# Performance work log

Measured on AMD Instinct MI355X. Metric: run time of the kernel, lower is better.

Reference implementation:

```python
import jax, jax.numpy as jnp
import numpy as np

N = 100000
E = 1600000
H = 128
L = 5
G = 128
OUT = 128
BN_EPS = 1e-5


def setup_inputs() -> dict:
    key = jax.random.key(0)
    ks = jax.random.split(key, 16)
    x = jax.random.randint(ks[0], (N,), 0, 1)
    edge_index = jax.random.randint(ks[1], (2, E), 0, N)
    edge_attr = jax.random.normal(ks[2], (E, 7), dtype=jnp.float32)
    batch = jnp.sort(jax.random.randint(ks[3], (N,), 0, G))
    s = 0.05
    node_emb = jax.random.normal(ks[4], (1, H), dtype=jnp.float32) * s
    W = jax.random.normal(ks[5], (L, H, H), dtype=jnp.float32) * s
    b = jnp.zeros((L, H), dtype=jnp.float32)
    We = jax.random.normal(ks[6], (L, 7, H), dtype=jnp.float32) * s
    be = jnp.zeros((L, H), dtype=jnp.float32)
    root = jax.random.normal(ks[7], (L, 1, H), dtype=jnp.float32) * s
    gamma = jnp.ones((L, H), dtype=jnp.float32)
    beta = jnp.zeros((L, H), dtype=jnp.float32)
    Wout = jax.random.normal(ks[8], (H, OUT), dtype=jnp.float32) * s
    bout = jnp.zeros((OUT,), dtype=jnp.float32)
    return {"x": x, "edge_index": edge_index, "edge_attr": edge_attr, "batch": batch,
            "node_emb": node_emb, "W": W, "b": b, "We": We, "be": be, "root": root,
            "gamma": gamma, "beta": beta, "Wout": Wout, "bout": bout}


def _batchnorm(h, g, bta):
    mu = jnp.mean(h, axis=0)
    var = jnp.var(h, axis=0)  # biased, as torch BN training normalization
    return (h - mu) * jax.lax.rsqrt(var + BN_EPS) * g + bta


def reference(x, edge_index, edge_attr, batch, node_emb, W, b, We, be, root, gamma, beta, Wout, bout):
    row, col = edge_index[0], edge_index[1]
    # degree(row) + 1
    deg = jax.ops.segment_sum(jnp.ones((E,), edge_attr.dtype), row, num_segments=N) + 1.0
    dis = deg ** -0.5  # never inf since deg >= 1
    norm = dis[row] * dis[col]  # [E]

    h = node_emb[x]  # [N, H]
    for i in range(L):
        xl = h @ W[i] + b[i]                    # [N, H]
        e = edge_attr @ We[i] + be[i]           # [E, H]
        msg = norm[:, None] * jax.nn.relu(xl[row] + e)   # [E, H]
        agg = jax.ops.segment_sum(msg, col, num_segments=N)
        h = agg + jax.nn.relu(xl + root[i]) / deg[:, None]
        h = _batchnorm(h, gamma[i], beta[i])
        if i < L - 1:
            h = jax.nn.relu(h)
    # global mean pool
    cnt = jax.ops.segment_sum(jnp.ones((N,), h.dtype), batch, num_segments=G)
    hg = jax.ops.segment_sum(h, batch, num_segments=G) / jnp.maximum(cnt, 1.0)[:, None]
    return hg @ Wout + bout
```

## Files before the change

kernel.cpp:

```cpp
#include <hip/hip_runtime.h>
#include <hip/hip_fp16.h>
#include <cstdint>
#include <cstddef>

#define N_NODES 100000
#define N_EDGES 1600000
#define H 128
#define L_LAYERS 5
#define G_GRAPHS 128
#define OUT_F 128
#define BN_EPS 1e-5f
#define SCAN_BLOCKS 98

typedef _Float16 half8_t __attribute__((ext_vector_type(8)));
typedef float floatx4 __attribute__((ext_vector_type(4)));

__device__ __forceinline__ float frelu(float x) { return fmaxf(x, 0.0f); }


__global__ void count_kernel(const int* __restrict__ erow, const int* __restrict__ ecol,
                             int* __restrict__ degcnt, int* __restrict__ hist) {
    int e = blockIdx.x * 256 + threadIdx.x;
    atomicAdd(&degcnt[erow[e]], 1);
    atomicAdd(&hist[ecol[e]], 1);
}

__global__ void finish_deg(const int* __restrict__ degcnt, float* __restrict__ dis,
                           float* __restrict__ invdeg) {
    int i = blockIdx.x * 256 + threadIdx.x;
    if (i < N_NODES) {
        float d = (float)degcnt[i] + 1.0f;
        dis[i] = rsqrtf(d);
        invdeg[i] = 1.0f / d;
    }
}

__global__ __launch_bounds__(1024) void scan_part(const int* __restrict__ hist,
                                                  int* __restrict__ rowptr,
                                                  int* __restrict__ blocksum) {
    int t = threadIdx.x;
    int i = blockIdx.x * 1024 + t;
    int orig = (i < N_NODES) ? hist[i] : 0;
    int v = orig;
#pragma unroll
    for (int off = 1; off < 64; off <<= 1) {
        int u = __shfl_up(v, off);
        if ((t & 63) >= off) v += u;
    }
    __shared__ int wsum[16];
    int wid = t >> 6;
    if ((t & 63) == 63) wsum[wid] = v;
    __syncthreads();
    int woff = 0;
#pragma unroll
    for (int w = 0; w < 16; w++)
        if (w < wid) woff += wsum[w];
    int incl = v + woff;
    if (i < N_NODES) rowptr[i] = incl - orig;
    if (t == 1023) blocksum[blockIdx.x] = incl;
}

__global__ __launch_bounds__(128) void scan_block(const int* __restrict__ blocksum,
                                                  int* __restrict__ blockoff,
                                                  int* __restrict__ rowptr) {
    int t = threadIdx.x;
    int orig = (t < SCAN_BLOCKS) ? blocksum[t] : 0;
    int v = orig;
#pragma unroll
    for (int off = 1; off < 64; off <<= 1) {
        int u = __shfl_up(v, off);
        if ((t & 63) >= off) v += u;
    }
    __shared__ int w0;
    if (t == 63) w0 = v;
    __syncthreads();
    if (t >= 64) v += w0;
    if (t < SCAN_BLOCKS) blockoff[t] = v - orig;
    if (t == 0) rowptr[N_NODES] = N_EDGES;
}

__global__ __launch_bounds__(1024) void scan_add(int* __restrict__ rowptr,
                                                 const int* __restrict__ blockoff,
                                                 int* __restrict__ cursor) {
    int i = blockIdx.x * 1024 + threadIdx.x;
    if (i < N_NODES) {
        int v = rowptr[i] + blockoff[blockIdx.x];
        rowptr[i] = v;
        cursor[i] = v;
    }
}

__global__ void scatter_kernel(const int* __restrict__ erow, const int* __restrict__ ecol,
                               const float* __restrict__ ea, const float* __restrict__ dis,
                               int* __restrict__ cursor,
                               float* __restrict__ ea8, int* __restrict__ rows) {
    int e = blockIdx.x * 256 + threadIdx.x;
    int c = ecol[e];
    int r = erow[e];
    float nrm = dis[r] * dis[c];
    int pos = atomicAdd(&cursor[c], 1);
    const float* p = ea + (size_t)e * 7;
    float a0 = p[0], a1 = p[1], a2 = p[2], a3 = p[3], a4 = p[4], a5 = p[5], a6 = p[6];
    float* dst = ea8 + (size_t)pos * 8;
    *(float4*)dst = make_float4(a0, a1, a2, a3);
    *(float4*)(dst + 4) = make_float4(a4, a5, a6, nrm);
    rows[pos] = r;
}

__global__ __launch_bounds__(256) void gemm_xl(const __half* __restrict__ hsrc,
                                               const int* __restrict__ xidx,
                                               const float* __restrict__ nemb,
                                               const float* __restrict__ colsum_p,
                                               const float* __restrict__ colsumsq_p,
                                               const float* __restrict__ gamma_p,
                                               const float* __restrict__ beta_p,
                                               const float* __restrict__ Wl,
                                               const float* __restrict__ bl,
                                               __half* __restrict__ xlo, int mode) {
    __shared__ half8_t sB[2048];
    __shared__ float sScale[H], sShift[H];
    int t = threadIdx.x;
    if (mode == 1 && t < H) {
        float mean = colsum_p[t] * (1.0f / N_NODES);
        float var = colsumsq_p[t] * (1.0f / N_NODES) - mean * mean;
        float s = gamma_p[t] * rsqrtf(var + BN_EPS);
        sScale[t] = s;
        sShift[t] = beta_p[t] - mean * s;
    }
    for (int idx = t; idx < 2048; idx += 256) {
        int ct = idx >> 8;
        int ks = (idx >> 6) & 3;
        int ln = idx & 63;
        int kbase = ks * 32 + (ln >> 4) * 8;
        int c = ct * 16 + (ln & 15);
        half8_t v;
#pragma unroll
        for (int i = 0; i < 8; i++)
            v[i] = (_Float16)Wl[(size_t)(kbase + i) * H + c];
        sB[idx] = v;
    }
    __syncthreads();

    int w = t >> 6, lane = t & 63;
    int lq = lane >> 4, lr = lane & 15;
    int rbase = blockIdx.x * 128 + w * 32;

    floatx4 acc[2][8];
#pragma unroll
    for (int rt = 0; rt < 2; rt++)
#pragma unroll
        for (int ct = 0; ct < 8; ct++) acc[rt][ct] = (floatx4)0.0f;

    float bias[8];
#pragma unroll
    for (int ct = 0; ct < 8; ct++) bias[ct] = bl[ct * 16 + lr];

    int arow[2], xv[2];
#pragma unroll
    for (int rt = 0; rt < 2; rt++) {
        int row = rbase + rt * 16 + lr;
        if (row > N_NODES - 1) row = N_NODES - 1;
        arow[rt] = row;
        if (mode == 0) xv[rt] = xidx[row];
    }

    for (int ks = 0; ks < 4; ks++) {
        int k0 = ks * 32 + lq * 8;
        half8_t a[2];
#pragma unroll
        for (int rt = 0; rt < 2; rt++) {
            float f[8];
            if (mode == 0) {
                const float* p = nemb + (size_t)xv[rt] * H + k0;
                float4 u0 = *(const float4*)p;
                float4 u1 = *(const float4*)(p + 4);
                f[0] = u0.x; f[1] = u0.y; f[2] = u0.z; f[3] = u0.w;
                f[4] = u1.x; f[5] = u1.y; f[6] = u1.z; f[7] = u1.w;
            } else {
                union { float4 f4; __half2 h2[4]; } u;
                u.f4 = *(const float4*)(hsrc + (size_t)arow[rt] * H + k0);
#pragma unroll
                for (int i = 0; i < 4; i++) {
                    float2 d = __half22float2(u.h2[i]);
                    f[2 * i] = d.x; f[2 * i + 1] = d.y;
                }
#pragma unroll
                for (int i = 0; i < 8; i++)
                    f[i] = frelu(f[i] * sScale[k0 + i] + sShift[k0 + i]);
            }
            half8_t av;
#pragma unroll
            for (int i = 0; i < 8; i++) av[i] = (_Float16)f[i];
            a[rt] = av;
        }
#pragma unroll
        for (int ct = 0; ct < 8; ct++) {
            half8_t bf = sB[(ct * 4 + ks) * 64 + lane];
            acc[0][ct] = __builtin_amdgcn_mfma_f32_16x16x32_f16(a[0], bf, acc[0][ct], 0, 0, 0);
            acc[1][ct] = __builtin_amdgcn_mfma_f32_16x16x32_f16(a[1], bf, acc[1][ct], 0, 0, 0);
        }
    }

#pragma unroll
    for (int rt = 0; rt < 2; rt++)
#pragma unroll
        for (int ct = 0; ct < 8; ct++)
#pragma unroll
            for (int r = 0; r < 4; r++) {
                int row = rbase + rt * 16 + lq * 4 + r;
                if (row < N_NODES)
                    xlo[(size_t)row * H + ct * 16 + lr] =
                        __float2half(acc[rt][ct][r] + bias[ct]);
            }
}

__global__ __launch_bounds__(256) void agg_kernel(
    const int* __restrict__ rowptr, const float* __restrict__ ea8,
    const int* __restrict__ rows, const __half2* __restrict__ xh2,
    const float* __restrict__ invdeg, const float* __restrict__ rootl,
    const float* __restrict__ Wel, const float* __restrict__ bel,
    __half2* __restrict__ hpreh, float* __restrict__ colsum,
    float* __restrict__ colsumsq) {
    int t = threadIdx.x;
    int lane = t & 63, wv = t >> 6;
    int c0 = lane * 2;
    float w00 = Wel[0 * H + c0], w01 = Wel[0 * H + c0 + 1];
    float w10 = Wel[1 * H + c0], w11 = Wel[1 * H + c0 + 1];
    float w20 = Wel[2 * H + c0], w21 = Wel[2 * H + c0 + 1];
    float w30 = Wel[3 * H + c0], w31 = Wel[3 * H + c0 + 1];
    float w40 = Wel[4 * H + c0], w41 = Wel[4 * H + c0 + 1];
    float w50 = Wel[5 * H + c0], w51 = Wel[5 * H + c0 + 1];
    float w60 = Wel[6 * H + c0], w61 = Wel[6 * H + c0 + 1];
    float be0 = bel[c0], be1 = bel[c0 + 1];
    float rt0 = rootl[c0], rt1 = rootl[c0 + 1];
    float s0 = 0, s1 = 0, q0 = 0, q1 = 0;

#define MLP_BODY(V0, V1, XG)                                                 \
    {                                                                        \
        float2 xg_ = __half22float2(XG);                                     \
        float m0_ = be0, m1_ = be1;                                          \
        m0_ = fmaf((V0).x, w00, m0_); m1_ = fmaf((V0).x, w01, m1_);          \
        m0_ = fmaf((V0).y, w10, m0_); m1_ = fmaf((V0).y, w11, m1_);          \
        m0_ = fmaf((V0).z, w20, m0_); m1_ = fmaf((V0).z, w21, m1_);          \
        m0_ = fmaf((V0).w, w30, m0_); m1_ = fmaf((V0).w, w31, m1_);          \
        m0_ = fmaf((V1).x, w40, m0_); m1_ = fmaf((V1).x, w41, m1_);          \
        m0_ = fmaf((V1).y, w50, m0_); m1_ = fmaf((V1).y, w51, m1_);          \
        m0_ = fmaf((V1).z, w60, m0_); m1_ = fmaf((V1).z, w61, m1_);          \
        a0 = fmaf(frelu(xg_.x + m0_), (V1).w, a0);                           \
        a1 = fmaf(frelu(xg_.y + m1_), (V1).w, a1);                           \
    }

    for (int n_ = blockIdx.x * 4 + wv; n_ < N_NODES; n_ += gridDim.x * 4) {
        int n = __builtin_amdgcn_readfirstlane(n_);
        int jb = __builtin_amdgcn_readfirstlane(rowptr[n]);
        int je = __builtin_amdgcn_readfirstlane(rowptr[n + 1]);
        float a0 = 0, a1 = 0;
        int j = jb;
        for (; j + 8 <= je; j += 8) {
            int rr[8];
#pragma unroll
            for (int i = 0; i < 8; i++) rr[i] = rows[j + i];
            __half2 g[8];
#pragma unroll
            for (int i = 0; i < 8; i++) g[i] = xh2[(size_t)rr[i] * 64 + lane];
#pragma unroll
            for (int i = 0; i < 8; i++) {
                const float* ep_ = ea8 + (size_t)(j + i) * 8;
                float4 va = *(const float4*)ep_, vb = *(const float4*)(ep_ + 4);
                MLP_BODY(va, vb, g[i]);
            }
        }
        if (j + 4 <= je) {
            int rr[4];
#pragma unroll
            for (int i = 0; i < 4; i++) rr[i] = rows[j + i];
            __half2 g[4];
#pragma unroll
            for (int i = 0; i < 4; i++) g[i] = xh2[(size_t)rr[i] * 64 + lane];
#pragma unroll
            for (int i = 0; i < 4; i++) {
                const float* ep_ = ea8 + (size_t)(j + i) * 8;
                float4 va = *(const float4*)ep_, vb = *(const float4*)(ep_ + 4);
                MLP_BODY(va, vb, g[i]);
            }
            j += 4;
        }
        for (; j < je; j++) {
            int r_ = rows[j];
            const float* ep_ = ea8 + (size_t)j * 8;
            float4 va = *(const float4*)ep_, vb = *(const float4*)(ep_ + 4);
            __half2 g_ = xh2[(size_t)r_ * 64 + lane];
            MLP_BODY(va, vb, g_);
        }
        float2 xn = __half22float2(xh2[(size_t)n * 64 + lane]);
        float id = invdeg[n];
        float p0 = a0 + frelu(xn.x + rt0) * id;
        float p1 = a1 + frelu(xn.y + rt1) * id;
        hpreh[(size_t)n * 64 + lane] = __float22half2_rn(make_float2(p0, p1));
        s0 += p0; s1 += p1;
        q0 = fmaf(p0, p0, q0); q1 = fmaf(p1, p1, q1);
    }
#undef MLP_BODY

    __shared__ float red[4][H];
    red[wv][c0] = s0; red[wv][c0 + 1] = s1;
    __syncthreads();
    if (wv == 0) {
        float t0 = red[0][c0] + red[1][c0] + red[2][c0] + red[3][c0];
        float t1 = red[0][c0 + 1] + red[1][c0 + 1] + red[2][c0 + 1] + red[3][c0 + 1];
        unsafeAtomicAdd(&colsum[c0], t0);
        unsafeAtomicAdd(&colsum[c0 + 1], t1);
    }
    __syncthreads();
    red[wv][c0] = q0; red[wv][c0 + 1] = q1;
    __syncthreads();
    if (wv == 0) {
        float t0 = red[0][c0] + red[1][c0] + red[2][c0] + red[3][c0];
        float t1 = red[0][c0 + 1] + red[1][c0 + 1] + red[2][c0 + 1] + red[3][c0 + 1];
        unsafeAtomicAdd(&colsumsq[c0], t0);
        unsafeAtomicAdd(&colsumsq[c0 + 1], t1);
    }
}

__global__ __launch_bounds__(256) void pool_kernel(const __half2* __restrict__ hh,
                                                   const int* __restrict__ batch,
                                                   const float* __restrict__ colsum_p,
                                                   const float* __restrict__ colsumsq_p,
                                                   const float* __restrict__ gamma_p,
                                                   const float* __restrict__ beta_p,
                                                   float* __restrict__ pooled,
                                                   float* __restrict__ cnt) {
    __shared__ float sScale[H], sShift[H];
    int t = threadIdx.x;
    if (t < H) {
        float mean = colsum_p[t] * (1.0f / N_NODES);
        float var = colsumsq_p[t] * (1.0f / N_NODES) - mean * mean;
        float s = gamma_p[t] * rsqrtf(var + BN_EPS);
        sScale[t] = s;
        sShift[t] = beta_p[t] - mean * s;
    }
    __syncthreads();
    int cg = t & 63, rg = t >> 6;
    int c0 = cg * 2;
    float sc0 = sScale[c0], sc1 = sScale[c0 + 1];
    float sh0 = sShift[c0], sh1 = sShift[c0 + 1];
    int per = (N_NODES + gridDim.x - 1) / gridDim.x;
    int rstart = blockIdx.x * per;
    int rend = min(rstart + per, N_NODES);
    float a0 = 0, a1 = 0, runc = 0.0f;
    int cur = -1;
    for (int rowi = rstart + rg; rowi < rend; rowi += 4) {
        int g = batch[rowi];
        if (g != cur) {
            if (cur >= 0) {
                unsafeAtomicAdd(&pooled[(size_t)cur * H + c0 + 0], a0);
                unsafeAtomicAdd(&pooled[(size_t)cur * H + c0 + 1], a1);
                if (cg == 0) unsafeAtomicAdd(&cnt[cur], runc);
            }
            cur = g; a0 = 0; a1 = 0; runc = 0.0f;
        }
        float2 v = __half22float2(hh[(size_t)rowi * 64 + cg]);
        a0 += v.x * sc0 + sh0;
        a1 += v.y * sc1 + sh1;
        runc += 1.0f;
    }
    if (cur >= 0) {
        unsafeAtomicAdd(&pooled[(size_t)cur * H + c0 + 0], a0);
        unsafeAtomicAdd(&pooled[(size_t)cur * H + c0 + 1], a1);
        if (cg == 0) unsafeAtomicAdd(&cnt[cur], runc);
    }
}

__global__ __launch_bounds__(128) void final_gemm(const float* __restrict__ pooled,
                                                  const float* __restrict__ cnt,
                                                  const float* __restrict__ Wout,
                                                  const float* __restrict__ bout,
                                                  float* __restrict__ out) {
    __shared__ float sh[H];
    int g = blockIdx.x;
    int o = threadIdx.x;
    float c = fmaxf(cnt[g], 1.0f);
    sh[o] = pooled[(size_t)g * H + o] / c;
    __syncthreads();
    float acc = bout[o];
#pragma unroll 8
    for (int k = 0; k < H; k++) acc += sh[k] * Wout[(size_t)k * OUT_F + o];
    out[(size_t)g * OUT_F + o] = acc;
}

extern "C" void kernel_launch(void* const* d_in, const int* in_sizes, int n_in,
                              void* d_out, int out_size, void* d_ws, size_t ws_size,
                              hipStream_t stream) {
    const int*   x     = (const int*)d_in[0];
    const int*   ei    = (const int*)d_in[1];
    const float* ea    = (const float*)d_in[2];
    const int*   batch = (const int*)d_in[3];
    const float* nemb  = (const float*)d_in[4];
    const float* W     = (const float*)d_in[5];
    const float* b     = (const float*)d_in[6];
    const float* We    = (const float*)d_in[7];
    const float* be    = (const float*)d_in[8];
    const float* root  = (const float*)d_in[9];
    const float* gamma = (const float*)d_in[10];
    const float* beta  = (const float*)d_in[11];
    const float* Wout  = (const float*)d_in[12];
    const float* bout  = (const float*)d_in[13];
    float* out = (float*)d_out;

    const int* erow = ei;
    const int* ecol = ei + N_EDGES;

    float* ws = (float*)d_ws;
    size_t NH = (size_t)N_NODES * H;
    float* ea8    = ws;
    int*   rows   = (int*)(ea8 + (size_t)N_EDGES * 8);
    float* hslot  = (float*)(rows + N_EDGES);
    __half* hpreh = (__half*)hslot;
    float* xslot  = hslot + NH / 2;
    __half* xlh   = (__half*)xslot;
    int*   rowptr = (int*)(xslot + NH / 2);
    float* dis    = (float*)(rowptr + N_NODES + 4);
    float* invdeg = dis + N_NODES;
    float* colsumAll = invdeg + N_NODES;
    float* pooled   = colsumAll + (size_t)L_LAYERS * 2 * H;
    float* cnt      = pooled + (size_t)G_GRAPHS * H;
    int*   blocksum = (int*)(cnt + G_GRAPHS);
    int*   blockoff = blocksum + 128;

    int* degcnt = (int*)hslot;
    int* hist   = degcnt + N_NODES;
    int* cursor = hist + N_NODES;

    hipMemsetAsync(degcnt, 0, 2 * N_NODES * sizeof(int), stream);
    hipMemsetAsync(colsumAll, 0, (size_t)L_LAYERS * 2 * H * sizeof(float), stream);
    hipLaunchKernelGGL(count_kernel, dim3(N_EDGES / 256), dim3(256), 0, stream,
                       erow, ecol, degcnt, hist);
    hipLaunchKernelGGL(finish_deg, dim3((N_NODES + 255) / 256), dim3(256), 0, stream,
                       degcnt, dis, invdeg);
    hipLaunchKernelGGL(scan_part, dim3(SCAN_BLOCKS), dim3(1024), 0, stream,
                       hist, rowptr, blocksum);
    hipLaunchKernelGGL(scan_block, dim3(1), dim3(128), 0, stream,
                       blocksum, blockoff, rowptr);
    hipLaunchKernelGGL(scan_add, dim3(SCAN_BLOCKS), dim3(1024), 0, stream,
                       rowptr, blockoff, cursor);
    hipLaunchKernelGGL(scatter_kernel, dim3(N_EDGES / 256), dim3(256), 0, stream,
                       erow, ecol, ea, dis, cursor, ea8, rows);

    for (int l = 0; l < L_LAYERS; l++) {
        const float* cs_prev = colsumAll + (size_t)(l - 1) * 2 * H;
        hipLaunchKernelGGL(gemm_xl, dim3((N_NODES + 127) / 128), dim3(256), 0, stream,
                           hpreh, x, nemb,
                           (l == 0) ? colsumAll : cs_prev,
                           (l == 0) ? colsumAll : cs_prev + H,
                           gamma + (size_t)(l ? l - 1 : 0) * H,
                           beta + (size_t)(l ? l - 1 : 0) * H,
                           W + (size_t)l * H * H, b + (size_t)l * H, xlh,
                           (l == 0) ? 0 : 1);
        float* cs = colsumAll + (size_t)l * 2 * H;
        hipLaunchKernelGGL(agg_kernel, dim3(2048), dim3(256), 0, stream,
                           rowptr, ea8, rows, (const __half2*)xlh, invdeg,
                           root + (size_t)l * H, We + (size_t)l * 7 * H, be + (size_t)l * H,
                           (__half2*)hpreh, cs, cs + H);
    }

    hipMemsetAsync(pooled, 0, ((size_t)G_GRAPHS * H + G_GRAPHS) * sizeof(float), stream);
    {
        const float* cs4 = colsumAll + (size_t)(L_LAYERS - 1) * 2 * H;
        hipLaunchKernelGGL(pool_kernel, dim3(256), dim3(256), 0, stream,
                           (const __half2*)hpreh, batch, cs4, cs4 + H,
                           gamma + (size_t)(L_LAYERS - 1) * H,
                           beta + (size_t)(L_LAYERS - 1) * H, pooled, cnt);
    }
    hipLaunchKernelGGL(final_gemm, dim3(G_GRAPHS), dim3(OUT_F), 0, stream,
                       pooled, cnt, Wout, bout, out);
}
```

Before: 1.365 ms.

## Assign contiguous node ranges per wave and software-pipeline edge gathers across nodes

The aggregation kernel now gives each wavefront a contiguous run of 13 nodes and walks their edges as one flat stream. It double-buffers the row indices and gathered xl features in batches of 8, prefetching the next batch while the current one is processed. A flush step emits each node's result at its boundary and prefetches the next node's self features. This removes per-node loop overhead and the serial tails for low-degree nodes, and keeps more gathers in flight, at the cost of more registers and per-edge boundary checks. 2048 blocks × 4 waves × 13 nodes covers all 100000 nodes.

```diff
diff --git a/kernel.cpp b/kernel.cpp
--- a/kernel.cpp
+++ b/kernel.cpp
@@ -11,6 +11,8 @@
 #define OUT_F 128
 #define BN_EPS 1e-5f
 #define SCAN_BLOCKS 98
+#define AGG_BLOCKS 2048
+#define NPW 13
 
 typedef _Float16 half8_t __attribute__((ext_vector_type(8)));
 typedef float floatx4 __attribute__((ext_vector_type(4)));
@@ -235,6 +237,27 @@
     float rt0 = rootl[c0], rt1 = rootl[c0 + 1];
     float s0 = 0, s1 = 0, q0 = 0, q1 = 0;
 
+    int wgid = blockIdx.x * 4 + wv;
+    int n0 = wgid * NPW;
+    bool active = (n0 < N_NODES);
+    int n1 = active ? min(n0 + NPW, N_NODES) : n0;
+    int n = n0;
+    float a0 = 0, a1 = 0;
+
+    __half2 xn_cur = __half2{}, xn_next = __half2{};
+    float idg_cur = 0, idg_next = 0;
+    int je = 0, e0 = 0, e1 = 0;
+    if (active) {
+        e0 = __builtin_amdgcn_readfirstlane(rowptr[n0]);
+        e1 = __builtin_amdgcn_readfirstlane(rowptr[n1]);
+        je = __builtin_amdgcn_readfirstlane(rowptr[n0 + 1]);
+        xn_cur = xh2[(size_t)n0 * 64 + lane];
+        idg_cur = invdeg[n0];
+        int nx = min(n0 + 1, N_NODES - 1);
+        xn_next = xh2[(size_t)nx * 64 + lane];
+        idg_next = invdeg[nx];
+    }
+
 #define MLP_BODY(V0, V1, XG)                                                 \
     {                                                                        \
         float2 xg_ = __half22float2(XG);                                     \
@@ -250,56 +273,87 @@
         a1 = fmaf(frelu(xg_.y + m1_), (V1).w, a1);                           \
     }
 
-    for (int n_ = blockIdx.x * 4 + wv; n_ < N_NODES; n_ += gridDim.x * 4) {
-        int n = __builtin_amdgcn_readfirstlane(n_);
-        int jb = __builtin_amdgcn_readfirstlane(rowptr[n]);
-        int je = __builtin_amdgcn_readfirstlane(rowptr[n + 1]);
-        float a0 = 0, a1 = 0;
-        int j = jb;
-        for (; j + 8 <= je; j += 8) {
-            int rr[8];
-#pragma unroll
-            for (int i = 0; i < 8; i++) rr[i] = rows[j + i];
-            __half2 g[8];
-#pragma unroll
-            for (int i = 0; i < 8; i++) g[i] = xh2[(size_t)rr[i] * 64 + lane];
-#pragma unroll
-            for (int i = 0; i < 8; i++) {
-                const float* ep_ = ea8 + (size_t)(j + i) * 8;
-                float4 va = *(const float4*)ep_, vb = *(const float4*)(ep_ + 4);
-                MLP_BODY(va, vb, g[i]);
+#define FLUSH()                                                              \
+    {                                                                        \
+        float2 xnf_ = __half22float2(xn_cur);                                \
+        float p0_ = a0 + frelu(xnf_.x + rt0) * idg_cur;                      \
+        float p1_ = a1 + frelu(xnf_.y + rt1) * idg_cur;                      \
+        hpreh[(size_t)n * 64 + lane] = __float22half2_rn(make_float2(p0_, p1_)); \
+        s0 += p0_; s1 += p1_;                                                \
+        q0 = fmaf(p0_, p0_, q0); q1 = fmaf(p1_, p1_, q1);                    \
+        a0 = 0; a1 = 0;                                                      \
+        xn_cur = xn_next; idg_cur = idg_next;                                \
+        int nn_ = min(n + 2, N_NODES - 1);                                   \
+        xn_next = xh2[(size_t)nn_ * 64 + lane];                              \
+        idg_next = invdeg[nn_];                                              \
+    }
+
+#define PROCESS(G)                                                           \
+    {                                                                        \
+        _Pragma("unroll")                                                    \
+        for (int i = 0; i < 8; i++) {                                        \
+            int jj = j + i;                                                  \
+            if (jj < e1) {                                                   \
+                while (jj >= je) {                                           \
+                    FLUSH();                                                 \
+                    n++;                                                     \
+                    je = __builtin_amdgcn_readfirstlane(rowptr[n + 1]);      \
+                }                                                            \
+                const float* ep_ = ea8 + (size_t)jj * 8;                     \
+                float4 va_ = *(const float4*)ep_;                            \
+                float4 vb_ = *(const float4*)(ep_ + 4);                      \
+                MLP_BODY(va_, vb_, G[i]);                                    \
+            }                                                                \
+        }                                                                    \
+    }
+
+    if (active && e1 > e0) {
+        int rrA[8], rrB[8];
+        __half2 gA[8], gB[8];
+        int eclamp = e1 - 1;
+#pragma unroll
+        for (int i = 0; i < 8; i++)
+            rrA[i] = __builtin_amdgcn_readfirstlane(rows[min(e0 + i, eclamp)]);
+#pragma unroll
+        for (int i = 0; i < 8; i++) gA[i] = xh2[(size_t)rrA[i] * 64 + lane];
+#pragma unroll
+        for (int i = 0; i < 8; i++)
+            rrB[i] = __builtin_amdgcn_readfirstlane(rows[min(e0 + 8 + i, eclamp)]);
+
+        int j = e0;
+        while (true) {
+            if (j >= e1) break;
+            {
+                if (j + 8 < e1) {
+#pragma unroll
+                    for (int i = 0; i < 8; i++) gB[i] = xh2[(size_t)rrB[i] * 64 + lane];
+#pragma unroll
+                    for (int i = 0; i < 8; i++)
+                        rrA[i] = __builtin_amdgcn_readfirstlane(rows[min(j + 16 + i, eclamp)]);
+                }
+                PROCESS(gA);
+                j += 8;
+            }
+            if (j >= e1) break;
+            {
+                if (j + 8 < e1) {
+#pragma unroll
+                    for (int i = 0; i < 8; i++) gA[i] = xh2[(size_t)rrA[i] * 64 + lane];
+#pragma unroll
+                    for (int i = 0; i < 8; i++)
+                        rrB[i] = __builtin_amdgcn_readfirstlane(rows[min(j + 16 + i, eclamp)]);
+                }
+                PROCESS(gB);
+                j += 8;
             }
         }
-        if (j + 4 <= je) {
-            int rr[4];
-#pragma unroll
-            for (int i = 0; i < 4; i++) rr[i] = rows[j + i];
-            __half2 g[4];
-#pragma unroll
-            for (int i = 0; i < 4; i++) g[i] = xh2[(size_t)rr[i] * 64 + lane];
-#pragma unroll
-            for (int i = 0; i < 4; i++) {
-                const float* ep_ = ea8 + (size_t)(j + i) * 8;
-                float4 va = *(const float4*)ep_, vb = *(const float4*)(ep_ + 4);
-                MLP_BODY(va, vb, g[i]);
-            }
-            j += 4;
-        }
-        for (; j < je; j++) {
-            int r_ = rows[j];
-            const float* ep_ = ea8 + (size_t)j * 8;
-            float4 va = *(const float4*)ep_, vb = *(const float4*)(ep_ + 4);
-            __half2 g_ = xh2[(size_t)r_ * 64 + lane];
-            MLP_BODY(va, vb, g_);
-        }
-        float2 xn = __half22float2(xh2[(size_t)n * 64 + lane]);
-        float id = invdeg[n];
-        float p0 = a0 + frelu(xn.x + rt0) * id;
-        float p1 = a1 + frelu(xn.y + rt1) * id;
-        hpreh[(size_t)n * 64 + lane] = __float22half2_rn(make_float2(p0, p1));
-        s0 += p0; s1 += p1;
-        q0 = fmaf(p0, p0, q0); q1 = fmaf(p1, p1, q1);
-    }
+    }
+    while (n < n1) {
+        FLUSH();
+        n++;
+    }
+#undef PROCESS
+#undef FLUSH
 #undef MLP_BODY
 
     __shared__ float red[4][H];
@@ -457,7 +511,7 @@
                            W + (size_t)l * H * H, b + (size_t)l * H, xlh,
                            (l == 0) ? 0 : 1);
         float* cs = colsumAll + (size_t)l * 2 * H;
-        hipLaunchKernelGGL(agg_kernel, dim3(2048), dim3(256), 0, stream,
+        hipLaunchKernelGGL(agg_kernel, dim3(AGG_BLOCKS), dim3(256), 0, stream,
                            rowptr, ea8, rows, (const __half2*)xlh, invdeg,
                            root + (size_t)l * H, We + (size_t)l * 7 * H, be + (size_t)l * H,
                            (__half2*)hpreh, cs, cs + H);
```

After: 1.724 ms. 1.26x slower.

## Pack edge attributes and norm into fp16, unroll aggregation loop to 16

Applied to the files above, without the earlier changes.

Edge attributes and the normalization factor are stored as eight fp16 values (16 bytes per edge) instead of eight fp32 values, halving the per-edge stream the aggregation kernel reads on every layer. The aggregation loop also adds a 16-edge unrolled stage so more neighbor-row gathers are in flight at once. The cost is fp16 rounding of edge features and norm, which lowers accuracy, plus higher register pressure from the wider unroll.

```diff
diff --git a/kernel.cpp b/kernel.cpp
--- a/kernel.cpp
+++ b/kernel.cpp
@@ -93,17 +93,19 @@
 __global__ void scatter_kernel(const int* __restrict__ erow, const int* __restrict__ ecol,
                                const float* __restrict__ ea, const float* __restrict__ dis,
                                int* __restrict__ cursor,
-                               float* __restrict__ ea8, int* __restrict__ rows) {
+                               float4* __restrict__ eah, int* __restrict__ rows) {
     int e = blockIdx.x * 256 + threadIdx.x;
     int c = ecol[e];
     int r = erow[e];
     float nrm = dis[r] * dis[c];
     int pos = atomicAdd(&cursor[c], 1);
     const float* p = ea + (size_t)e * 7;
-    float a0 = p[0], a1 = p[1], a2 = p[2], a3 = p[3], a4 = p[4], a5 = p[5], a6 = p[6];
-    float* dst = ea8 + (size_t)pos * 8;
-    *(float4*)dst = make_float4(a0, a1, a2, a3);
-    *(float4*)(dst + 4) = make_float4(a4, a5, a6, nrm);
+    union { float4 f4; __half2 h2[4]; } u;
+    u.h2[0] = __float22half2_rn(make_float2(p[0], p[1]));
+    u.h2[1] = __float22half2_rn(make_float2(p[2], p[3]));
+    u.h2[2] = __float22half2_rn(make_float2(p[4], p[5]));
+    u.h2[3] = __float22half2_rn(make_float2(p[6], nrm));
+    eah[pos] = u.f4;
     rows[pos] = r;
 }
 
@@ -215,7 +217,7 @@
 }
 
 __global__ __launch_bounds__(256) void agg_kernel(
-    const int* __restrict__ rowptr, const float* __restrict__ ea8,
+    const int* __restrict__ rowptr, const float4* __restrict__ eah,
     const int* __restrict__ rows, const __half2* __restrict__ xh2,
     const float* __restrict__ invdeg, const float* __restrict__ rootl,
     const float* __restrict__ Wel, const float* __restrict__ bel,
@@ -235,19 +237,24 @@
     float rt0 = rootl[c0], rt1 = rootl[c0 + 1];
     float s0 = 0, s1 = 0, q0 = 0, q1 = 0;
 
-#define MLP_BODY(V0, V1, XG)                                                 \
+#define MLP_BODY(PV, XG)                                                     \
     {                                                                        \
+        const __half2* ph_ = (const __half2*)&(PV);                          \
+        float2 A01_ = __half22float2(ph_[0]);                                \
+        float2 A23_ = __half22float2(ph_[1]);                                \
+        float2 A45_ = __half22float2(ph_[2]);                                \
+        float2 A6N_ = __half22float2(ph_[3]);                                \
         float2 xg_ = __half22float2(XG);                                     \
         float m0_ = be0, m1_ = be1;                                          \
-        m0_ = fmaf((V0).x, w00, m0_); m1_ = fmaf((V0).x, w01, m1_);          \
-        m0_ = fmaf((V0).y, w10, m0_); m1_ = fmaf((V0).y, w11, m1_);          \
-        m0_ = fmaf((V0).z, w20, m0_); m1_ = fmaf((V0).z, w21, m1_);          \
-        m0_ = fmaf((V0).w, w30, m0_); m1_ = fmaf((V0).w, w31, m1_);          \
-        m0_ = fmaf((V1).x, w40, m0_); m1_ = fmaf((V1).x, w41, m1_);          \
-        m0_ = fmaf((V1).y, w50, m0_); m1_ = fmaf((V1).y, w51, m1_);          \
-        m0_ = fmaf((V1).z, w60, m0_); m1_ = fmaf((V1).z, w61, m1_);          \
-        a0 = fmaf(frelu(xg_.x + m0_), (V1).w, a0);                           \
-        a1 = fmaf(frelu(xg_.y + m1_), (V1).w, a1);                           \
+        m0_ = fmaf(A01_.x, w00, m0_); m1_ = fmaf(A01_.x, w01, m1_);          \
+        m0_ = fmaf(A01_.y, w10, m0_); m1_ = fmaf(A01_.y, w11, m1_);          \
+        m0_ = fmaf(A23_.x, w20, m0_); m1_ = fmaf(A23_.x, w21, m1_);          \
+        m0_ = fmaf(A23_.y, w30, m0_); m1_ = fmaf(A23_.y, w31, m1_);          \
+        m0_ = fmaf(A45_.x, w40, m0_); m1_ = fmaf(A45_.x, w41, m1_);          \
+        m0_ = fmaf(A45_.y, w50, m0_); m1_ = fmaf(A45_.y, w51, m1_);          \
+        m0_ = fmaf(A6N_.x, w60, m0_); m1_ = fmaf(A6N_.x, w61, m1_);          \
+        a0 = fmaf(frelu(xg_.x + m0_), A6N_.y, a0);                           \
+        a1 = fmaf(frelu(xg_.y + m1_), A6N_.y, a1);                           \
     }
 
     for (int n_ = blockIdx.x * 4 + wv; n_ < N_NODES; n_ += gridDim.x * 4) {
@@ -256,7 +263,20 @@
         int je = __builtin_amdgcn_readfirstlane(rowptr[n + 1]);
         float a0 = 0, a1 = 0;
         int j = jb;
-        for (; j + 8 <= je; j += 8) {
+        for (; j + 16 <= je; j += 16) {
+            int rr[16];
+#pragma unroll
+            for (int i = 0; i < 16; i++) rr[i] = rows[j + i];
+            __half2 g[16];
+#pragma unroll
+            for (int i = 0; i < 16; i++) g[i] = xh2[(size_t)rr[i] * 64 + lane];
+#pragma unroll
+            for (int i = 0; i < 16; i++) {
+                float4 pv = eah[j + i];
+                MLP_BODY(pv, g[i]);
+            }
+        }
+        if (j + 8 <= je) {
             int rr[8];
 #pragma unroll
             for (int i = 0; i < 8; i++) rr[i] = rows[j + i];
@@ -265,10 +285,10 @@
             for (int i = 0; i < 8; i++) g[i] = xh2[(size_t)rr[i] * 64 + lane];
 #pragma unroll
             for (int i = 0; i < 8; i++) {
-                const float* ep_ = ea8 + (size_t)(j + i) * 8;
-                float4 va = *(const float4*)ep_, vb = *(const float4*)(ep_ + 4);
-                MLP_BODY(va, vb, g[i]);
-            }
+                float4 pv = eah[j + i];
+                MLP_BODY(pv, g[i]);
+            }
+            j += 8;
         }
         if (j + 4 <= je) {
             int rr[4];
@@ -279,18 +299,16 @@
             for (int i = 0; i < 4; i++) g[i] = xh2[(size_t)rr[i] * 64 + lane];
 #pragma unroll
             for (int i = 0; i < 4; i++) {
-                const float* ep_ = ea8 + (size_t)(j + i) * 8;
-                float4 va = *(const float4*)ep_, vb = *(const float4*)(ep_ + 4);
-                MLP_BODY(va, vb, g[i]);
+                float4 pv = eah[j + i];
+                MLP_BODY(pv, g[i]);
             }
             j += 4;
         }
         for (; j < je; j++) {
             int r_ = rows[j];
-            const float* ep_ = ea8 + (size_t)j * 8;
-            float4 va = *(const float4*)ep_, vb = *(const float4*)(ep_ + 4);
             __half2 g_ = xh2[(size_t)r_ * 64 + lane];
-            MLP_BODY(va, vb, g_);
+            float4 pv = eah[j];
+            MLP_BODY(pv, g_);
         }
         float2 xn = __half22float2(xh2[(size_t)n * 64 + lane]);
         float id = invdeg[n];
@@ -412,8 +430,8 @@
 
     float* ws = (float*)d_ws;
     size_t NH = (size_t)N_NODES * H;
-    float* ea8    = ws;
-    int*   rows   = (int*)(ea8 + (size_t)N_EDGES * 8);
+    float4* eah   = (float4*)ws;
+    int*   rows   = (int*)(eah + N_EDGES);
     float* hslot  = (float*)(rows + N_EDGES);
     __half* hpreh = (__half*)hslot;
     float* xslot  = hslot + NH / 2;
@@ -444,7 +462,7 @@
     hipLaunchKernelGGL(scan_add, dim3(SCAN_BLOCKS), dim3(1024), 0, stream,
                        rowptr, blockoff, cursor);
     hipLaunchKernelGGL(scatter_kernel, dim3(N_EDGES / 256), dim3(256), 0, stream,
-                       erow, ecol, ea, dis, cursor, ea8, rows);
+                       erow, ecol, ea, dis, cursor, eah, rows);
 
     for (int l = 0; l < L_LAYERS; l++) {
         const float* cs_prev = colsumAll + (size_t)(l - 1) * 2 * H;
@@ -458,7 +476,7 @@
                            (l == 0) ? 0 : 1);
         float* cs = colsumAll + (size_t)l * 2 * H;
         hipLaunchKernelGGL(agg_kernel, dim3(2048), dim3(256), 0, stream,
-                           rowptr, ea8, rows, (const __half2*)xlh, invdeg,
+                           rowptr, eah, rows, (const __half2*)xlh, invdeg,
                            root + (size_t)l * H, We + (size_t)l * 7 * H, be + (size_t)l * H,
                            (__half2*)hpreh, cs, cs + H);
     }
```

After: 1.316 ms. 1.04x faster.
